# Kernel optimization log

Measured on AMD Instinct MI355X. Metric: run time of the kernel, lower is better.

Reference implementation:

```python
import jax, jax.numpy as jnp
import numpy as np

SOCIAL_IDS = (1, 18)
BN_EPS = 1e-5


def conv1d(x, w, b):
    # x: [N, C, L], w: [O, I, 3], padding=1
    y = jax.lax.conv_general_dilated(x, w, window_strides=(1,), padding=[(1, 1)],
                                     dimension_numbers=("NCH", "OIH", "NCH"))
    return y + b[None, :, None]


def batchnorm(x, gamma, beta):
    # training-mode BatchNorm1d: biased stats over (N, L)
    m = x.mean(axis=(0, 2), keepdims=True)
    v = ((x - m) ** 2).mean(axis=(0, 2), keepdims=True)
    return gamma[None, :, None] * (x - m) * jax.lax.rsqrt(v + BN_EPS) + beta[None, :, None]


def social_stats(activity_ids):
    # Vectorized run-length-encoding of the social mask (replaces the per-element Python loop).
    mask = (activity_ids == SOCIAL_IDS[0]) | (activity_ids == SOCIAL_IDS[1])  # [B, S]
    prev = jnp.pad(mask[:, :-1], ((0, 0), (1, 0)))
    starts = mask & ~prev
    nseg = starts.sum(-1).astype(jnp.float32)                 # sigma_frequency
    total_dur = mask.sum(-1).astype(jnp.float32)
    mu_dur = jnp.where(nseg > 0, total_dur / jnp.maximum(nseg, 1.0), 0.0)
    # gap positions: non-social with social both before and after -> exactly the inter-segment gaps
    cum = jnp.cumsum(mask, axis=-1)
    rcum = jnp.cumsum(mask[:, ::-1], axis=-1)[:, ::-1]
    gap_sum = ((~mask) & (cum > 0) & (rcum > 0)).sum(-1).astype(jnp.float32)
    resp = jnp.where(nseg > 1, gap_sum / jnp.maximum(nseg - 1.0, 1.0), 0.0)
    return jnp.stack([mu_dur, nseg, resp], axis=-1)          # [B, 3]


def compute_sws(cur, base):
    num = cur[:, 0] * cur[:, 1]
    den = base[:, 0] * base[:, 1] + 1e-10
    return jnp.clip(1.0 - num / den, 0.0, 1.0)


def setup_inputs() -> dict:
    key = jax.random.key(0)
    ks = jax.random.split(key, 16)
    B, S, D, V = 32, 8192, 128, 21
    inp = {
        "activity_ids": jax.random.randint(ks[0], (B, S), 0, V),
        "baseline_stats": jax.random.uniform(ks[1], (B, 3), dtype=jnp.float32) * 10.0 + 0.5,
        "embed": jax.random.normal(ks[2], (V, D), dtype=jnp.float32),
        "W1": jax.random.normal(ks[3], (256, D, 3), dtype=jnp.float32) * 0.05,
        "b1": jnp.zeros((256,), jnp.float32),
        "g1": jnp.ones((256,), jnp.float32),
        "be1": jnp.zeros((256,), jnp.float32),
        "W2": jax.random.normal(ks[4], (128, 256, 3), dtype=jnp.float32) * 0.05,
        "b2": jnp.zeros((128,), jnp.float32),
        "g2": jnp.ones((128,), jnp.float32),
        "be2": jnp.zeros((128,), jnp.float32),
        "W3": jax.random.normal(ks[5], (D, 128, 3), dtype=jnp.float32) * 0.05,
        "b3": jnp.zeros((D,), jnp.float32),
        "Ws": jax.random.normal(ks[6], (D, 3), dtype=jnp.float32) * 0.1,
        "bs": jnp.zeros((D,), jnp.float32),
        "Wo": jax.random.normal(ks[7], (D, 2 * D), dtype=jnp.float32) * 0.05,
        "bo": jnp.zeros((D,), jnp.float32),
    }
    return inp


def reference(activity_ids, baseline_stats, embed, W1, b1, g1, be1, W2, b2, g2, be2,
              W3, b3, Ws, bs, Wo, bo):
    x = embed[activity_ids]                   # [B, S, D]
    x = x.transpose(0, 2, 1)                  # [B, D, S]
    x = jax.nn.relu(batchnorm(conv1d(x, W1, b1), g1, be1))
    x = jax.nn.relu(batchnorm(conv1d(x, W2, b2), g2, be2))
    x = jax.nn.relu(conv1d(x, W3, b3))
    h_cnn = x.mean(axis=2)                    # [B, D]
    stats = social_stats(activity_ids)        # [B, 3]
    h_stats = stats @ Ws.T + bs               # [B, D]
    sws = compute_sws(stats, baseline_stats)  # [B]
    h = jnp.concatenate([h_cnn, h_stats], axis=-1)
    h_si = h @ Wo.T + bo                      # [B, D]
    return (h_si, sws)
```

## Files before the change

### kernel.cpp

```cpp
#include <hip/hip_runtime.h>
#include <hip/hip_bf16.h>
#include <cstdint>
#include <cstddef>

#define B_    32
#define S_    8192
#define D_    128
#define V_    21
#define VP_   22
#define T_    (VP_*VP_*VP_)
#define TPAD_ 10656
#define C1_   256
#define C2_   128
#define NPOS_ (B_*S_)
#define NCHUNK_ 128

using bf16x8 = __attribute__((ext_vector_type(8))) short;
using f32x4  = __attribute__((ext_vector_type(4))) float;
using u32x4  = __attribute__((ext_vector_type(4))) unsigned;

__device__ inline unsigned short f2bf(float f) {
  union { float f; unsigned u; } v; v.f = f;
  unsigned r = v.u + 0x7fffu + ((v.u >> 16) & 1u);
  return (unsigned short)(r >> 16);
}
__device__ inline float bf2f(unsigned short h) {
  union { unsigned u; float f; } v; v.u = ((unsigned)h) << 16; return v.f;
}

__global__ void k_prep(const float* __restrict__ W1, const float* __restrict__ emb,
                       const float* __restrict__ W2, const float* __restrict__ W3,
                       float* __restrict__ G, unsigned short* __restrict__ Wr2,
                       unsigned short* __restrict__ W3r) {
  int bid = blockIdx.x;
  if (bid < 66) {
    int v = bid % VP_, k = bid / VP_, o = threadIdx.x;
    __shared__ float e[D_];
    if (o < D_) e[o] = (v < V_) ? emb[v * D_ + o] : 0.f;
    __syncthreads();
    float acc = 0.f;
    if (v < V_) {
      for (int i = 0; i < D_; ++i) acc += W1[o * (D_ * 3) + i * 3 + k] * e[i];
    }
    G[(k * VP_ + v) * C1_ + o] = acc;
  } else {
    int idx = (bid - 66) * 256 + threadIdx.x;
    if (idx < 384 * 256) {
      int r = idx >> 8, o = idx & 255;
      int k = r >> 7, p = r & 127;
      Wr2[idx] = f2bf(W2[(p * C1_ + o) * 3 + k]);
    } else {
      int j = idx - 384 * 256;
      if (j < 128 * 384) {
        int q = j / 384, kk = j % 384;
        int k = kk >> 7, p = kk & 127;
        W3r[q * 384 + kk] = f2bf(W3[(q * C2_ + p) * 3 + k]);
      }
    }
  }
}

__global__ void k_tidx_social(const int* __restrict__ ids, int* __restrict__ tIdx,
                              int* __restrict__ cnt, int* __restrict__ socC,
                              int* __restrict__ socS, int* __restrict__ socF,
                              int* __restrict__ socL) {
  int idx = blockIdx.x * 256 + threadIdx.x;
  int b = idx >> 13, s = idx & (S_ - 1);
  const int* row = ids + b * S_;
  int a = (s > 0)      ? row[s - 1] : V_;
  int m = row[s];
  int c = (s < S_ - 1) ? row[s + 1] : V_;
  int t = (a * VP_ + m) * VP_ + c;
  tIdx[idx] = t;
  atomicAdd(&cnt[t], 1);

  bool sm = (m == 1) | (m == 18);
  bool pm = (a == 1) | (a == 18);
  unsigned long long bm = __ballot(sm);
  unsigned long long bs = __ballot(sm && !pm);
  __shared__ int l0, l1, l2, l3;
  if (threadIdx.x == 0) { l0 = 0; l1 = 0; l2 = 0; l3 = 0; }
  __syncthreads();
  int lane = threadIdx.x & 63;
  int fc = sm ? (S_ - 1 - s) : 0;
  int lv = sm ? s : 0;
#pragma unroll
  for (int off = 1; off < 64; off <<= 1) {
    fc = max(fc, __shfl_xor(fc, off));
    lv = max(lv, __shfl_xor(lv, off));
  }
  if (lane == 0) {
    atomicAdd(&l0, (int)__popcll(bm));
    atomicAdd(&l1, (int)__popcll(bs));
    atomicMax(&l2, fc);
    atomicMax(&l3, lv);
  }
  __syncthreads();
  if (threadIdx.x == 0) {
    atomicAdd(&socC[b], l0); atomicAdd(&socS[b], l1);
    atomicMax(&socF[b], l2); atomicMax(&socL[b], l3);
  }
}

__global__ void k_stats1(const float* __restrict__ G, const float* __restrict__ b1,
                         const int* __restrict__ cnt,
                         float* __restrict__ m1acc, float* __restrict__ v1acc) {
  int o = threadIdx.x;
  float bb = b1[o];
  float s = 0.f, sq = 0.f;
  int t0 = blockIdx.x * 16;
#pragma unroll 4
  for (int i = 0; i < 16; ++i) {
    int t = t0 + i;
    if (t >= T_) break;
    int a = t / (VP_ * VP_), m = (t / VP_) % VP_, c = t % VP_;
    float x = G[a * C1_ + o] + G[(VP_ + m) * C1_ + o] + G[(2 * VP_ + c) * C1_ + o] + bb;
    float w = (float)cnt[t];
    s += w * x; sq += w * x * x;
  }
  atomicAdd(&m1acc[o], s);
  atomicAdd(&v1acc[o], sq);
}

__global__ void k_z1(const float* __restrict__ G, const float* __restrict__ b1,
                     const float* __restrict__ m1a, const float* __restrict__ v1a,
                     const float* __restrict__ g1, const float* __restrict__ be1,
                     unsigned* __restrict__ Z1u) {
  int tid = threadIdx.x;
  int t = blockIdx.x * 2 + (tid >> 7);
  int o = (tid & 127) * 2;
  float m0 = m1a[o] * (1.f / NPOS_), m1v = m1a[o + 1] * (1.f / NPOS_);
  float a0 = g1[o]     * rsqrtf(v1a[o]     * (1.f / NPOS_) - m0 * m0   + 1e-5f);
  float a1 = g1[o + 1] * rsqrtf(v1a[o + 1] * (1.f / NPOS_) - m1v * m1v + 1e-5f);
  float c0 = be1[o] - m0 * a0, c1 = be1[o + 1] - m1v * a1;
  unsigned pk = 0;
  if (t < T_) {
    int a = t / (VP_ * VP_), m = (t / VP_) % VP_, c = t % VP_;
    float2 xa = *(const float2*)(G + (size_t)a * C1_ + o);
    float2 xm = *(const float2*)(G + (size_t)(VP_ + m) * C1_ + o);
    float2 xc = *(const float2*)(G + (size_t)(2 * VP_ + c) * C1_ + o);
    float x0 = xa.x + xm.x + xc.x + b1[o];
    float x1 = xa.y + xm.y + xc.y + b1[o + 1];
    float z0 = fmaxf(a0 * x0 + c0, 0.f);
    float z1 = fmaxf(a1 * x1 + c1, 0.f);
    pk = (unsigned)f2bf(z0) | ((unsigned)f2bf(z1) << 16);
  }
  Z1u[(size_t)t * 128 + (tid & 127)] = pk;
}

__global__ void __launch_bounds__(256) k_hgemm(const unsigned short* __restrict__ Z1,
                                               const unsigned short* __restrict__ Wr2,
                                               unsigned short* __restrict__ H) {
  int wave = threadIdx.x >> 6, lane = threadIdx.x & 63;
  int mt = blockIdx.x * 4 + wave;
  if (mt >= TPAD_ / 16) return;
  int nt0 = blockIdx.y * 4;
  int rc   = lane & 15;
  int kgrp = lane >> 4;
  bf16x8 af[8];
  const unsigned short* Arow = Z1 + (size_t)(mt * 16 + rc) * C1_ + kgrp * 8;
#pragma unroll
  for (int st = 0; st < 8; ++st) af[st] = *(const bf16x8*)(Arow + st * 32);
#pragma unroll
  for (int ntp = 0; ntp < 2; ++ntp) {
    int ntA = nt0 + ntp * 2, ntB = ntA + 1;
    f32x4 accA = {0.f, 0.f, 0.f, 0.f}, accB = {0.f, 0.f, 0.f, 0.f};
    const unsigned short* BrA = Wr2 + (size_t)(ntA * 16 + rc) * C1_ + kgrp * 8;
    const unsigned short* BrB = Wr2 + (size_t)(ntB * 16 + rc) * C1_ + kgrp * 8;
#pragma unroll
    for (int st = 0; st < 8; ++st) {
      bf16x8 bA = *(const bf16x8*)(BrA + st * 32);
      bf16x8 bB = *(const bf16x8*)(BrB + st * 32);
      accA = __builtin_amdgcn_mfma_f32_16x16x32_bf16(af[st], bA, accA, 0, 0, 0);
      accB = __builtin_amdgcn_mfma_f32_16x16x32_bf16(af[st], bB, accB, 0, 0, 0);
    }
#pragma unroll
    for (int r = 0; r < 4; ++r) {
      int m = mt * 16 + kgrp * 4 + r;
      H[(size_t)m * 384 + ntA * 16 + rc] = f2bf(accA[r]);
      H[(size_t)m * 384 + ntB * 16 + rc] = f2bf(accB[r]);
    }
  }
}

#define YPB 256
__global__ void __launch_bounds__(256, 3) k_y2stats(const int* __restrict__ tIdx,
        const unsigned short* __restrict__ H, const float* __restrict__ b2,
        unsigned short* __restrict__ y2, float* __restrict__ sum, float* __restrict__ sq) {
  int lane16 = threadIdx.x & 15;
  int pgrp   = threadIdx.x >> 4;
  int base0  = blockIdx.x * YPB;
  float bb[8];
  const float* b2s = b2 + lane16 * 8;
#pragma unroll
  for (int j = 0; j < 8; ++j) bb[j] = b2s[j];
  float sAcc[8] = {0,0,0,0,0,0,0,0}, qAcc[8] = {0,0,0,0,0,0,0,0};

  for (int ib = 0; ib < 2; ++ib) {
    int base = base0 + ib * 128;
    int tA[8], tM[8], tC[8];
#pragma unroll
    for (int i = 0; i < 8; ++i) {
      int pos = base + i * 16 + pgrp;
      int s = pos & (S_ - 1);
      const int* tr = tIdx + (pos & ~(S_ - 1));
      tM[i] = tr[s];
      int sa = s > 0 ? s - 1 : 0;
      int sc = s < S_ - 1 ? s + 1 : s;
      int ta = tr[sa], tc = tr[sc];
      tA[i] = (s > 0)      ? ta : T_;
      tC[i] = (s < S_ - 1) ? tc : T_;
    }
    bf16x8 h0[8], h1[8], h2[8];
#pragma unroll
    for (int i = 0; i < 8; ++i)
      h1[i] = *(const bf16x8*)(H + (size_t)tM[i] * 384 + 128 + lane16 * 8);
#pragma unroll
    for (int i = 0; i < 8; ++i)
      h0[i] = *(const bf16x8*)(H + (size_t)tA[i] * 384 +   0 + lane16 * 8);
#pragma unroll
    for (int i = 0; i < 8; ++i)
      h2[i] = *(const bf16x8*)(H + (size_t)tC[i] * 384 + 256 + lane16 * 8);

#pragma unroll
    for (int i = 0; i < 8; ++i) {
      int pos = base + i * 16 + pgrp;
      float y[8];
#pragma unroll
      for (int j = 0; j < 8; ++j) {
        y[j] = bb[j] + bf2f((unsigned short)h0[i][j]) + bf2f((unsigned short)h1[i][j])
                     + bf2f((unsigned short)h2[i][j]);
        sAcc[j] += y[j]; qAcc[j] += y[j] * y[j];
      }
      u32x4 pk;
      pk[0] = (unsigned)f2bf(y[0]) | ((unsigned)f2bf(y[1]) << 16);
      pk[1] = (unsigned)f2bf(y[2]) | ((unsigned)f2bf(y[3]) << 16);
      pk[2] = (unsigned)f2bf(y[4]) | ((unsigned)f2bf(y[5]) << 16);
      pk[3] = (unsigned)f2bf(y[6]) | ((unsigned)f2bf(y[7]) << 16);
      *(u32x4*)(y2 + (size_t)pos * C2_ + lane16 * 8) = pk;
    }
  }

  __shared__ float ls[128], lq[128];
  if (threadIdx.x < 128) { ls[threadIdx.x] = 0.f; lq[threadIdx.x] = 0.f; }
  __syncthreads();
  int lane = threadIdx.x & 63;
#pragma unroll
  for (int j = 0; j < 8; ++j) {
    float v = sAcc[j], q = qAcc[j];
    v += __shfl_xor(v, 16); v += __shfl_xor(v, 32);
    q += __shfl_xor(q, 16); q += __shfl_xor(q, 32);
    if (lane < 16) { atomicAdd(&ls[lane16 * 8 + j], v); atomicAdd(&lq[lane16 * 8 + j], q); }
  }
  __syncthreads();
  if (threadIdx.x < 128) {
    atomicAdd(&sum[threadIdx.x], ls[threadIdx.x]);
    atomicAdd(&sq[threadIdx.x],  lq[threadIdx.x]);
  }
}

#define CH_ 64
__global__ void __launch_bounds__(256, 6) k_conv3(const unsigned short* __restrict__ y2,
      const float* __restrict__ s2a, const float* __restrict__ q2a,
      const float* __restrict__ g2, const float* __restrict__ be2,
      const unsigned short* __restrict__ W3r, const float* __restrict__ b3,
      float* __restrict__ part) {
  __shared__ unsigned short z2s[66 * 128];
  int b     = blockIdx.x >> 7;
  int chunk = blockIdx.x & 127;
  int s0    = chunk * CH_;
  int tid = threadIdx.x;

  {
    int lane16 = tid & 15;
    int rowg   = tid >> 4;
    const unsigned short* ybase = y2 + (size_t)b * S_ * C2_ + lane16 * 8;
    bf16x8 hv[5];
    int uu[5];
#pragma unroll
    for (int it = 0; it < 5; ++it) {
      int pos = (it < 4) ? (it * 16 + rowg) : (64 + (rowg & 1));
      int u = s0 - 1 + pos;
      uu[it] = u;
      int uc = min(max(u, 0), S_ - 1);
      hv[it] = *(const bf16x8*)(ybase + (size_t)uc * C2_);
    }
    float aa[8], cc[8];
#pragma unroll
    for (int j = 0; j < 8; ++j) {
      int ch = lane16 * 8 + j;
      float mm = s2a[ch] * (1.f / NPOS_);
      float vv = q2a[ch] * (1.f / NPOS_) - mm * mm;
      float a  = g2[ch] * rsqrtf(vv + 1e-5f);
      aa[j] = a; cc[j] = be2[ch] - mm * a;
    }
#pragma unroll
    for (int it = 0; it < 5; ++it) {
      int pos = (it < 4) ? (it * 16 + rowg) : (64 + (rowg & 1));
      bool valid = (uu[it] >= 0) & (uu[it] < S_);
      float z[8];
#pragma unroll
      for (int j = 0; j < 8; ++j)
        z[j] = fmaxf(aa[j] * bf2f((unsigned short)hv[it][j]) + cc[j], 0.f);
      u32x4 pk;
      pk[0] = (unsigned)f2bf(z[0]) | ((unsigned)f2bf(z[1]) << 16);
      pk[1] = (unsigned)f2bf(z[2]) | ((unsigned)f2bf(z[3]) << 16);
      pk[2] = (unsigned)f2bf(z[4]) | ((unsigned)f2bf(z[5]) << 16);
      pk[3] = (unsigned)f2bf(z[6]) | ((unsigned)f2bf(z[7]) << 16);
      if (!valid) pk = (u32x4){0, 0, 0, 0};
      if (it < 4 || rowg < 2) {
        int byte = (lane16 * 16) ^ ((pos & 7) << 4);
        *(u32x4*)((char*)z2s + pos * 256 + byte) = pk;
      }
    }
  }
  __syncthreads();

  int qp = tid >> 6, lane = tid & 63;
  int rc = lane & 15, kgrp = lane >> 4;
  f32x4 acc[2][4];
#pragma unroll
  for (int qt = 0; qt < 2; ++qt)
#pragma unroll
    for (int n = 0; n < 4; ++n) acc[qt][n] = (f32x4){0.f, 0.f, 0.f, 0.f};

  const unsigned short* A0 = W3r + (size_t)(qp * 32 +  0 + rc) * 384 + kgrp * 8;
  const unsigned short* A1 = W3r + (size_t)(qp * 32 + 16 + rc) * 384 + kgrp * 8;
#pragma unroll
  for (int st = 0; st < 12; ++st) {
    bf16x8 a0 = *(const bf16x8*)(A0 + st * 32);
    bf16x8 a1 = *(const bf16x8*)(A1 + st * 32);
    int k = st >> 2, pb = st & 3;
    int pbyte = (pb * 32 + kgrp * 8) * 2;
    bf16x8 bfr[4];
#pragma unroll
    for (int ntl = 0; ntl < 4; ++ntl) {
      int pos  = ntl * 16 + rc + k;
      int byte = pbyte ^ ((pos & 7) << 4);
      bfr[ntl] = *(const bf16x8*)((const char*)z2s + pos * 256 + byte);
    }
#pragma unroll
    for (int ntl = 0; ntl < 4; ++ntl) {
      acc[0][ntl] = __builtin_amdgcn_mfma_f32_16x16x32_bf16(a0, bfr[ntl], acc[0][ntl], 0, 0, 0);
      acc[1][ntl] = __builtin_amdgcn_mfma_f32_16x16x32_bf16(a1, bfr[ntl], acc[1][ntl], 0, 0, 0);
    }
  }

#pragma unroll
  for (int qt = 0; qt < 2; ++qt) {
    float partial[4];
    float b3q[4];
#pragma unroll
    for (int r = 0; r < 4; ++r) {
      b3q[r] = b3[qp * 32 + qt * 16 + kgrp * 4 + r];
      partial[r] = 0.f;
    }
#pragma unroll
    for (int ntl = 0; ntl < 4; ++ntl)
#pragma unroll
      for (int r = 0; r < 4; ++r)
        partial[r] += fmaxf(acc[qt][ntl][r] + b3q[r], 0.f);
#pragma unroll
    for (int r = 0; r < 4; ++r) {
      float v = partial[r];
      v += __shfl_xor(v, 1); v += __shfl_xor(v, 2);
      v += __shfl_xor(v, 4); v += __shfl_xor(v, 8);
      if (rc == 0) {
        int q = qp * 32 + qt * 16 + kgrp * 4 + r;
        part[((size_t)b * C2_ + q) * NCHUNK_ + chunk] = v;
      }
    }
  }
}

__global__ void k_final(const float* __restrict__ part,
      const int* __restrict__ socC, const int* __restrict__ socS,
      const int* __restrict__ socF, const int* __restrict__ socL,
      const float* __restrict__ baseline,
      const float* __restrict__ Ws, const float* __restrict__ bs,
      const float* __restrict__ Wo, const float* __restrict__ bo,
      float* __restrict__ out) {
  int b = blockIdx.x, q = threadIdx.x;
  __shared__ float h[256];
  __shared__ float st3[3];
  {
    const float4* p4 = (const float4*)(part + ((size_t)b * C2_ + q) * NCHUNK_);
    float acc = 0.f;
#pragma unroll 8
    for (int i = 0; i < NCHUNK_ / 4; ++i) {
      float4 v = p4[i];
      acc += v.x + v.y + v.z + v.w;
    }
    h[q] = acc * (1.f / S_);
  }
  if (q == 0) {
    float total = (float)socC[b], nseg = (float)socS[b];
    int first = (S_ - 1) - socF[b], last = socL[b];
    float mu   = (nseg > 0.f) ? total / fmaxf(nseg, 1.f) : 0.f;
    float gap  = (nseg > 0.f) ? (float)(last - first + 1) - total : 0.f;
    float resp = (nseg > 1.f) ? gap / fmaxf(nseg - 1.f, 1.f) : 0.f;
    st3[0] = mu; st3[1] = nseg; st3[2] = resp;
    float den = baseline[b * 3 + 0] * baseline[b * 3 + 1] + 1e-10f;
    float sws = 1.f - mu * nseg / den;
    out[B_ * C2_ + b] = fminf(fmaxf(sws, 0.f), 1.f);
  }
  __syncthreads();
  h[128 + q] = Ws[q * 3] * st3[0] + Ws[q * 3 + 1] * st3[1] + Ws[q * 3 + 2] * st3[2] + bs[q];
  __syncthreads();
  float acc = bo[q];
  const float4* Wo4 = (const float4*)(Wo + q * 256);
#pragma unroll 8
  for (int j4 = 0; j4 < 64; ++j4) {
    float4 wv = Wo4[j4];
    acc += wv.x * h[j4 * 4] + wv.y * h[j4 * 4 + 1] + wv.z * h[j4 * 4 + 2] + wv.w * h[j4 * 4 + 3];
  }
  out[b * C2_ + q] = acc;
}

extern "C" void kernel_launch(void* const* d_in, const int* in_sizes, int n_in,
                              void* d_out, int out_size, void* d_ws, size_t ws_size,
                              hipStream_t stream) {
  const int*   ids = (const int*)  d_in[0];
  const float* bas = (const float*)d_in[1];
  const float* emb = (const float*)d_in[2];
  const float* W1  = (const float*)d_in[3];
  const float* b1  = (const float*)d_in[4];
  const float* g1  = (const float*)d_in[5];
  const float* be1 = (const float*)d_in[6];
  const float* W2  = (const float*)d_in[7];
  const float* b2  = (const float*)d_in[8];
  const float* g2  = (const float*)d_in[9];
  const float* be2 = (const float*)d_in[10];
  const float* W3  = (const float*)d_in[11];
  const float* b3  = (const float*)d_in[12];
  const float* Ws  = (const float*)d_in[13];
  const float* bs  = (const float*)d_in[14];
  const float* Wo  = (const float*)d_in[15];
  const float* bo  = (const float*)d_in[16];
  float* out = (float*)d_out;

  char* w = (char*)d_ws;
  size_t off = 0;
  auto alloc = [&](size_t bytes) -> size_t {
    size_t o = off; off = (off + bytes + 255) & ~(size_t)255; return o;
  };
  size_t o_cnt  = alloc(T_ * 4);
  size_t o_m1   = alloc(C1_ * 4);
  size_t o_v1   = alloc(C1_ * 4);
  size_t o_s2   = alloc(C2_ * 4);
  size_t o_q2   = alloc(C2_ * 4);
  size_t o_socC = alloc(B_ * 4);
  size_t o_socS = alloc(B_ * 4);
  size_t o_socF = alloc(B_ * 4);
  size_t o_socL = alloc(B_ * 4);
  size_t zeroEnd = off;
  size_t o_part = alloc((size_t)B_ * C2_ * NCHUNK_ * 4);
  size_t o_tidx = alloc((size_t)NPOS_ * 4);
  size_t o_G    = alloc((size_t)3 * VP_ * C1_ * 4);
  size_t o_Z1   = alloc((size_t)TPAD_ * C1_ * 2);
  size_t o_Wr2  = alloc((size_t)384 * 256 * 2);
  size_t o_W3r  = alloc((size_t)128 * 384 * 2);
  size_t o_H    = alloc((size_t)TPAD_ * 384 * 2);
  size_t o_y2   = alloc((size_t)NPOS_ * C2_ * 2);
  (void)ws_size; (void)n_in; (void)in_sizes; (void)out_size;

  int*            cnt  = (int*)(w + o_cnt);
  float*          m1a  = (float*)(w + o_m1);
  float*          v1a  = (float*)(w + o_v1);
  float*          s2a  = (float*)(w + o_s2);
  float*          q2a  = (float*)(w + o_q2);
  int*            socC = (int*)(w + o_socC);
  int*            socS = (int*)(w + o_socS);
  int*            socF = (int*)(w + o_socF);
  int*            socL = (int*)(w + o_socL);
  float*          part = (float*)(w + o_part);
  int*            tIdx = (int*)(w + o_tidx);
  float*          G    = (float*)(w + o_G);
  unsigned short* Z1   = (unsigned short*)(w + o_Z1);
  unsigned short* Wr2  = (unsigned short*)(w + o_Wr2);
  unsigned short* W3r  = (unsigned short*)(w + o_W3r);
  unsigned short* H    = (unsigned short*)(w + o_H);
  unsigned short* y2   = (unsigned short*)(w + o_y2);

  hipMemsetAsync(w, 0, zeroEnd, stream);

  k_prep       <<<66 + 768, 256, 0, stream>>>(W1, emb, W2, W3, G, Wr2, W3r);
  k_tidx_social<<<NPOS_ / 256, 256, 0, stream>>>(ids, tIdx, cnt, socC, socS, socF, socL);
  k_stats1     <<<(T_ + 15) / 16, 256, 0, stream>>>(G, b1, cnt, m1a, v1a);
  k_z1         <<<TPAD_ / 2, 256, 0, stream>>>(G, b1, m1a, v1a, g1, be1, (unsigned*)Z1);
  k_hgemm      <<<dim3((TPAD_ / 16 + 3) / 4, 6), 256, 0, stream>>>(Z1, Wr2, H);
  k_y2stats    <<<NPOS_ / YPB, 256, 0, stream>>>(tIdx, H, b2, y2, s2a, q2a);
  k_conv3      <<<B_ * NCHUNK_, 256, 0, stream>>>(y2, s2a, q2a, g2, be2, W3r, b3, part);
  k_final      <<<B_, 128, 0, stream>>>(part, socC, socS, socF, socL, bas, Ws, bs, Wo, bo, out);
}
```

Measured before the change: 291.7 us.

## Enlarge conv3 position chunks and remap waves to positions; widen hgemm N tiles

k_conv3 now handles 128 positions per block instead of 64, so half as many blocks run and the halo overhead per position drops. Each wave now owns 32 positions and computes all 128 output channels, reading W3 fragments straight from global/L1 for each qt. A shared-memory cross-wave reduction writes the partials in a chunk-major layout, and k_final reads them strided. k_hgemm gives each block 8 N-tiles instead of 4, which halves grid.y and reuses the A fragments more; the cost is more registers and lower occupancy (conv3 launch bounds go from 6 to 4 blocks per SM).

```diff
diff --git a/kernel.cpp b/kernel.cpp
--- a/kernel.cpp
+++ b/kernel.cpp
@@ -13,7 +13,8 @@
 #define C1_   256
 #define C2_   128
 #define NPOS_ (B_*S_)
-#define NCHUNK_ 128
+#define CH_   128
+#define NCHUNK_ 64
 
 using bf16x8 = __attribute__((ext_vector_type(8))) short;
 using f32x4  = __attribute__((ext_vector_type(4))) float;
@@ -154,7 +155,7 @@
   int wave = threadIdx.x >> 6, lane = threadIdx.x & 63;
   int mt = blockIdx.x * 4 + wave;
   if (mt >= TPAD_ / 16) return;
-  int nt0 = blockIdx.y * 4;
+  int nt0 = blockIdx.y * 8;
   int rc   = lane & 15;
   int kgrp = lane >> 4;
   bf16x8 af[8];
@@ -162,7 +163,7 @@
 #pragma unroll
   for (int st = 0; st < 8; ++st) af[st] = *(const bf16x8*)(Arow + st * 32);
 #pragma unroll
-  for (int ntp = 0; ntp < 2; ++ntp) {
+  for (int ntp = 0; ntp < 4; ++ntp) {
     int ntA = nt0 + ntp * 2, ntB = ntA + 1;
     f32x4 accA = {0.f, 0.f, 0.f, 0.f}, accB = {0.f, 0.f, 0.f, 0.f};
     const unsigned short* BrA = Wr2 + (size_t)(ntA * 16 + rc) * C1_ + kgrp * 8;
@@ -259,15 +260,14 @@
   }
 }
 
-#define CH_ 64
-__global__ void __launch_bounds__(256, 6) k_conv3(const unsigned short* __restrict__ y2,
+__global__ void __launch_bounds__(256, 4) k_conv3(const unsigned short* __restrict__ y2,
       const float* __restrict__ s2a, const float* __restrict__ q2a,
       const float* __restrict__ g2, const float* __restrict__ be2,
       const unsigned short* __restrict__ W3r, const float* __restrict__ b3,
       float* __restrict__ part) {
-  __shared__ unsigned short z2s[66 * 128];
-  int b     = blockIdx.x >> 7;
-  int chunk = blockIdx.x & 127;
+  __shared__ unsigned short z2s[130 * 128];
+  int b     = blockIdx.x >> 6;
+  int chunk = blockIdx.x & 63;
   int s0    = chunk * CH_;
   int tid = threadIdx.x;
 
@@ -275,11 +275,11 @@
     int lane16 = tid & 15;
     int rowg   = tid >> 4;
     const unsigned short* ybase = y2 + (size_t)b * S_ * C2_ + lane16 * 8;
-    bf16x8 hv[5];
-    int uu[5];
-#pragma unroll
-    for (int it = 0; it < 5; ++it) {
-      int pos = (it < 4) ? (it * 16 + rowg) : (64 + (rowg & 1));
+    bf16x8 hv[9];
+    int uu[9];
+#pragma unroll
+    for (int it = 0; it < 9; ++it) {
+      int pos = it * 16 + rowg;
       int u = s0 - 1 + pos;
       uu[it] = u;
       int uc = min(max(u, 0), S_ - 1);
@@ -295,8 +295,8 @@
       aa[j] = a; cc[j] = be2[ch] - mm * a;
     }
 #pragma unroll
-    for (int it = 0; it < 5; ++it) {
-      int pos = (it < 4) ? (it * 16 + rowg) : (64 + (rowg & 1));
+    for (int it = 0; it < 9; ++it) {
+      int pos = it * 16 + rowg;
       bool valid = (uu[it] >= 0) & (uu[it] < S_);
       float z[8];
 #pragma unroll
@@ -308,68 +308,62 @@
       pk[2] = (unsigned)f2bf(z[4]) | ((unsigned)f2bf(z[5]) << 16);
       pk[3] = (unsigned)f2bf(z[6]) | ((unsigned)f2bf(z[7]) << 16);
       if (!valid) pk = (u32x4){0, 0, 0, 0};
-      if (it < 4 || rowg < 2) {
-        int byte = (lane16 * 16) ^ ((pos & 7) << 4);
+      if (pos < CH_ + 2) {
+        int byte = (lane16 * 16) ^ ((pos & 15) << 4);
         *(u32x4*)((char*)z2s + pos * 256 + byte) = pk;
       }
     }
   }
   __syncthreads();
 
-  int qp = tid >> 6, lane = tid & 63;
+  int wave = tid >> 6, lane = tid & 63;
   int rc = lane & 15, kgrp = lane >> 4;
-  f32x4 acc[2][4];
-#pragma unroll
-  for (int qt = 0; qt < 2; ++qt)
-#pragma unroll
-    for (int n = 0; n < 4; ++n) acc[qt][n] = (f32x4){0.f, 0.f, 0.f, 0.f};
-
-  const unsigned short* A0 = W3r + (size_t)(qp * 32 +  0 + rc) * 384 + kgrp * 8;
-  const unsigned short* A1 = W3r + (size_t)(qp * 32 + 16 + rc) * 384 + kgrp * 8;
+  f32x4 acc[8][2];
+#pragma unroll
+  for (int qt = 0; qt < 8; ++qt) {
+    acc[qt][0] = (f32x4){0.f, 0.f, 0.f, 0.f};
+    acc[qt][1] = (f32x4){0.f, 0.f, 0.f, 0.f};
+  }
+  const unsigned short* Wbase = W3r + (size_t)rc * 384 + kgrp * 8;
 #pragma unroll
   for (int st = 0; st < 12; ++st) {
-    bf16x8 a0 = *(const bf16x8*)(A0 + st * 32);
-    bf16x8 a1 = *(const bf16x8*)(A1 + st * 32);
     int k = st >> 2, pb = st & 3;
-    int pbyte = (pb * 32 + kgrp * 8) * 2;
-    bf16x8 bfr[4];
-#pragma unroll
-    for (int ntl = 0; ntl < 4; ++ntl) {
-      int pos  = ntl * 16 + rc + k;
-      int byte = pbyte ^ ((pos & 7) << 4);
-      bfr[ntl] = *(const bf16x8*)((const char*)z2s + pos * 256 + byte);
-    }
-#pragma unroll
-    for (int ntl = 0; ntl < 4; ++ntl) {
-      acc[0][ntl] = __builtin_amdgcn_mfma_f32_16x16x32_bf16(a0, bfr[ntl], acc[0][ntl], 0, 0, 0);
-      acc[1][ntl] = __builtin_amdgcn_mfma_f32_16x16x32_bf16(a1, bfr[ntl], acc[1][ntl], 0, 0, 0);
-    }
-  }
-
-#pragma unroll
-  for (int qt = 0; qt < 2; ++qt) {
-    float partial[4];
-    float b3q[4];
-#pragma unroll
-    for (int r = 0; r < 4; ++r) {
-      b3q[r] = b3[qp * 32 + qt * 16 + kgrp * 4 + r];
-      partial[r] = 0.f;
-    }
-#pragma unroll
-    for (int ntl = 0; ntl < 4; ++ntl)
-#pragma unroll
-      for (int r = 0; r < 4; ++r)
-        partial[r] += fmaxf(acc[qt][ntl][r] + b3q[r], 0.f);
-#pragma unroll
-    for (int r = 0; r < 4; ++r) {
-      float v = partial[r];
-      v += __shfl_xor(v, 1); v += __shfl_xor(v, 2);
-      v += __shfl_xor(v, 4); v += __shfl_xor(v, 8);
-      if (rc == 0) {
-        int q = qp * 32 + qt * 16 + kgrp * 4 + r;
-        part[((size_t)b * C2_ + q) * NCHUNK_ + chunk] = v;
-      }
-    }
+    int pbyte = pb * 64 + kgrp * 16;
+    int pos0 = (wave * 2) * 16 + rc + k;
+    int pos1 = pos0 + 16;
+    bf16x8 bfr0 = *(const bf16x8*)((const char*)z2s + pos0 * 256 + (pbyte ^ ((pos0 & 15) << 4)));
+    bf16x8 bfr1 = *(const bf16x8*)((const char*)z2s + pos1 * 256 + (pbyte ^ ((pos1 & 15) << 4)));
+#pragma unroll
+    for (int qt = 0; qt < 8; ++qt) {
+      bf16x8 af = *(const bf16x8*)(Wbase + (size_t)qt * 16 * 384 + st * 32);
+      acc[qt][0] = __builtin_amdgcn_mfma_f32_16x16x32_bf16(af, bfr0, acc[qt][0], 0, 0, 0);
+      acc[qt][1] = __builtin_amdgcn_mfma_f32_16x16x32_bf16(af, bfr1, acc[qt][1], 0, 0, 0);
+    }
+  }
+
+  __syncthreads();
+  float* red = (float*)z2s;
+#pragma unroll
+  for (int qt = 0; qt < 8; ++qt) {
+    const float4 b3q = *(const float4*)(b3 + qt * 16 + kgrp * 4);
+    float p0 = fmaxf(acc[qt][0][0] + b3q.x, 0.f) + fmaxf(acc[qt][1][0] + b3q.x, 0.f);
+    float p1 = fmaxf(acc[qt][0][1] + b3q.y, 0.f) + fmaxf(acc[qt][1][1] + b3q.y, 0.f);
+    float p2 = fmaxf(acc[qt][0][2] + b3q.z, 0.f) + fmaxf(acc[qt][1][2] + b3q.z, 0.f);
+    float p3 = fmaxf(acc[qt][0][3] + b3q.w, 0.f) + fmaxf(acc[qt][1][3] + b3q.w, 0.f);
+#pragma unroll
+    for (int off = 1; off < 16; off <<= 1) {
+      p0 += __shfl_xor(p0, off); p1 += __shfl_xor(p1, off);
+      p2 += __shfl_xor(p2, off); p3 += __shfl_xor(p3, off);
+    }
+    if (rc == 0) {
+      float* r4 = red + wave * 128 + qt * 16 + kgrp * 4;
+      r4[0] = p0; r4[1] = p1; r4[2] = p2; r4[3] = p3;
+    }
+  }
+  __syncthreads();
+  if (tid < 128) {
+    float v = red[tid] + red[128 + tid] + red[256 + tid] + red[384 + tid];
+    part[((size_t)b * NCHUNK_ + chunk) * C2_ + tid] = v;
   }
 }
 
@@ -384,13 +378,10 @@
   __shared__ float h[256];
   __shared__ float st3[3];
   {
-    const float4* p4 = (const float4*)(part + ((size_t)b * C2_ + q) * NCHUNK_);
     float acc = 0.f;
+    const float* pb = part + (size_t)b * NCHUNK_ * C2_ + q;
 #pragma unroll 8
-    for (int i = 0; i < NCHUNK_ / 4; ++i) {
-      float4 v = p4[i];
-      acc += v.x + v.y + v.z + v.w;
-    }
+    for (int i = 0; i < NCHUNK_; ++i) acc += pb[i * C2_];
     h[q] = acc * (1.f / S_);
   }
   if (q == 0) {
@@ -454,7 +445,7 @@
   size_t o_socF = alloc(B_ * 4);
   size_t o_socL = alloc(B_ * 4);
   size_t zeroEnd = off;
-  size_t o_part = alloc((size_t)B_ * C2_ * NCHUNK_ * 4);
+  size_t o_part = alloc((size_t)B_ * NCHUNK_ * C2_ * 4);
   size_t o_tidx = alloc((size_t)NPOS_ * 4);
   size_t o_G    = alloc((size_t)3 * VP_ * C1_ * 4);
   size_t o_Z1   = alloc((size_t)TPAD_ * C1_ * 2);
@@ -488,7 +479,7 @@
   k_tidx_social<<<NPOS_ / 256, 256, 0, stream>>>(ids, tIdx, cnt, socC, socS, socF, socL);
   k_stats1     <<<(T_ + 15) / 16, 256, 0, stream>>>(G, b1, cnt, m1a, v1a);
   k_z1         <<<TPAD_ / 2, 256, 0, stream>>>(G, b1, m1a, v1a, g1, be1, (unsigned*)Z1);
-  k_hgemm      <<<dim3((TPAD_ / 16 + 3) / 4, 6), 256, 0, stream>>>(Z1, Wr2, H);
+  k_hgemm      <<<dim3((TPAD_ / 16 + 3) / 4, 3), 256, 0, stream>>>(Z1, Wr2, H);
   k_y2stats    <<<NPOS_ / YPB, 256, 0, stream>>>(tIdx, H, b2, y2, s2a, q2a);
   k_conv3      <<<B_ * NCHUNK_, 256, 0, stream>>>(y2, s2a, q2a, g2, be2, W3r, b3, part);
   k_final      <<<B_, 128, 0, stream>>>(part, socC, socS, socF, socL, bas, Ws, bs, Wo, bo, out);
```

Result: slower. 335.8 us (+15.1%).
